# Kernel tuning notes

Hardware: AMD Instinct MI355X
Metric: run time of the kernel (lower is better)

Reference implementation:

```python
import jax, jax.numpy as jnp
import numpy as np

B, S, D, H = 2, 2048, 1024, 16
HD = D // H  # head dim 64

def setup_inputs() -> dict:
    key = jax.random.key(0)
    ks = jax.random.split(key, 12)
    s = 1.0 / np.sqrt(D)
    return {
        "query": jax.random.normal(ks[0], (B, S, D), jnp.float32),
        "key": jax.random.normal(ks[1], (B, S, D), jnp.float32),
        "value": jax.random.normal(ks[2], (B, S, D), jnp.float32),
        "Wq": jax.random.normal(ks[3], (D, D), jnp.float32) * s,
        "bq": jnp.zeros((D,), jnp.float32),
        "Wk": jax.random.normal(ks[4], (D, D), jnp.float32) * s,
        "bk": jnp.zeros((D,), jnp.float32),
        "Wv": jax.random.normal(ks[5], (D, D), jnp.float32) * s,
        "bv": jnp.zeros((D,), jnp.float32),
        "Wo": jax.random.normal(ks[6], (D, D), jnp.float32) * s,
        "bo": jnp.zeros((D,), jnp.float32),
    }

def _split_heads(x):
    # [B,S,D] -> [B,H,S,HD]
    return x.reshape(B, -1, H, HD).transpose(0, 2, 1, 3)

def reference(query, key, value, Wq, bq, Wk, bk, Wv, bv, Wo, bo):
    q = _split_heads(query @ Wq + bq)
    k = _split_heads(key @ Wk + bk)
    v = _split_heads(value @ Wv + bv)
    scale = 1.0 / np.sqrt(HD).astype(np.float32)
    scores = jnp.einsum('bhqd,bhkd->bhqk', q, k) * scale  # [B,H,S,S]
    attn = jax.nn.softmax(scores, axis=-1)
    ctx = jnp.einsum('bhqk,bhkd->bhqd', attn, v)  # [B,H,S,HD]
    ctx = ctx.transpose(0, 2, 1, 3).reshape(B, -1, D)
    out = ctx @ Wo + bo
    return out, attn
```

## Files before the change

### kernel.cpp

```cpp
#include <hip/hip_runtime.h>

#define B_ 2
#define S_ 2048
#define D_ 1024
#define H_ 16
#define HD_ 64

typedef float f32x4 __attribute__((ext_vector_type(4)));
typedef short s16x8 __attribute__((ext_vector_type(8)));

#define MFMA16(a, b, c) __builtin_amdgcn_mfma_f32_16x16x32_bf16((a), (b), (c), 0, 0, 0)

__device__ __forceinline__ unsigned short bf16_rne(float f) {
    unsigned int u = __float_as_uint(f);
    u += 0x7FFFu + ((u >> 16) & 1u);
    return (unsigned short)(u >> 16);
}
__device__ __forceinline__ float bf16_f32(unsigned short h) {
    return __uint_as_float(((unsigned int)h) << 16);
}
__device__ __forceinline__ void split_bf16(float x, short& hi, short& lo) {
    unsigned short h = bf16_rne(x);
    float r = x - bf16_f32(h);
    hi = (short)h;
    lo = (short)bf16_rne(r);
}

__global__ void wt_split_kernel(const float* __restrict__ W0, const float* __restrict__ W1,
                                const float* __restrict__ W2, const float* __restrict__ W3,
                                short* __restrict__ WtHi, short* __restrict__ WtLo) {
    int z = blockIdx.z;
    const float* W = (z == 0) ? W0 : (z == 1) ? W1 : (z == 2) ? W2 : W3;
    short* Hi = WtHi + (size_t)z * 1048576;
    short* Lo = WtLo + (size_t)z * 1048576;
    __shared__ float tile[32][33];
    int n0 = blockIdx.x * 32, k0 = blockIdx.y * 32;
    int c = threadIdx.x & 31, r = threadIdx.x >> 5;
#pragma unroll
    for (int i = 0; i < 4; i++) {
        int kl = r + i * 8;
        tile[kl][c] = W[(size_t)(k0 + kl) * D_ + n0 + c];
    }
    __syncthreads();
#pragma unroll
    for (int i = 0; i < 4; i++) {
        int nl = r + i * 8;
        float v = tile[c][nl];
        short h, l;
        split_bf16(v, h, l);
        size_t idx = (size_t)(n0 + nl) * D_ + k0 + c;
        Hi[idx] = h;
        Lo[idx] = l;
    }
}

__global__ __launch_bounds__(256) void proj_kernel(
    const float* __restrict__ Xq, const float* __restrict__ Xk, const float* __restrict__ Xv,
    const float* __restrict__ bq, const float* __restrict__ bk, const float* __restrict__ bv,
    const short* __restrict__ WtHi, const short* __restrict__ WtLo,
    short* __restrict__ Qhi, short* __restrict__ Qlo,
    short* __restrict__ Khi, short* __restrict__ Klo,
    short* __restrict__ VtHi, short* __restrict__ VtLo) {
    int z = blockIdx.z;
    const float* X = (z == 0) ? Xq : (z == 1) ? Xk : Xv;
    const float* bias = (z == 0) ? bq : (z == 1) ? bk : bv;
    const short* BH = WtHi + (size_t)z * 1048576;
    const short* BL = WtLo + (size_t)z * 1048576;
    int n0 = blockIdx.x * 64, m0 = blockIdx.y * 64;

    __shared__ alignas(16) short Ah[64][40], Al[64][40], Bh[64][40], Bl[64][40];

    int tid = threadIdx.x;
    int lane = tid & 63, w = tid >> 6;
    int wm = (w >> 1) * 32, wn = (w & 1) * 32;
    int quad = lane >> 4, l15 = lane & 15;

    f32x4 acc[2][2] = {};
    int sr = tid >> 2, scol = (tid & 3) * 8;

    for (int kb = 0; kb < 32; kb++) {
        int k0 = kb * 32;
        const float* src = X + (size_t)(m0 + sr) * D_ + k0 + scol;
        float4 f0 = *(const float4*)(src);
        float4 f1 = *(const float4*)(src + 4);
        float v[8] = {f0.x, f0.y, f0.z, f0.w, f1.x, f1.y, f1.z, f1.w};
        s16x8 hi8, lo8;
#pragma unroll
        for (int i = 0; i < 8; i++) {
            short h, l;
            split_bf16(v[i], h, l);
            hi8[i] = h;
            lo8[i] = l;
        }
        *(s16x8*)&Ah[sr][scol] = hi8;
        *(s16x8*)&Al[sr][scol] = lo8;
        *(s16x8*)&Bh[sr][scol] = *(const s16x8*)(BH + (size_t)(n0 + sr) * D_ + k0 + scol);
        *(s16x8*)&Bl[sr][scol] = *(const s16x8*)(BL + (size_t)(n0 + sr) * D_ + k0 + scol);
        __syncthreads();

        s16x8 ah[2], al[2], bh[2], bl[2];
#pragma unroll
        for (int mi = 0; mi < 2; mi++) {
            int m = wm + mi * 16 + l15;
            ah[mi] = *(const s16x8*)&Ah[m][quad * 8];
            al[mi] = *(const s16x8*)&Al[m][quad * 8];
        }
#pragma unroll
        for (int ni = 0; ni < 2; ni++) {
            int n = wn + ni * 16 + l15;
            bh[ni] = *(const s16x8*)&Bh[n][quad * 8];
            bl[ni] = *(const s16x8*)&Bl[n][quad * 8];
        }
#pragma unroll
        for (int mi = 0; mi < 2; mi++)
#pragma unroll
            for (int ni = 0; ni < 2; ni++) {
                acc[mi][ni] = MFMA16(ah[mi], bh[ni], acc[mi][ni]);
                acc[mi][ni] = MFMA16(ah[mi], bl[ni], acc[mi][ni]);
                acc[mi][ni] = MFMA16(al[mi], bh[ni], acc[mi][ni]);
            }
        __syncthreads();
    }

#pragma unroll
    for (int mi = 0; mi < 2; mi++)
#pragma unroll
        for (int ni = 0; ni < 2; ni++) {
            int nglob = n0 + wn + ni * 16 + l15;
            float bb = bias[nglob];
#pragma unroll
            for (int r = 0; r < 4; r++) {
                int mglob = m0 + wm + mi * 16 + quad * 4 + r;
                float cv = acc[mi][ni][r] + bb;
                short h, l;
                split_bf16(cv, h, l);
                if (z == 2) {
                    int bidx = mglob >> 11, s = mglob & 2047;
                    int hh = nglob >> 6, d = nglob & 63;
                    size_t idx = ((size_t)((bidx * H_ + hh) * HD_ + d)) * S_ + s;
                    VtHi[idx] = h;
                    VtLo[idx] = l;
                } else if (z == 0) {
                    size_t idx = (size_t)mglob * D_ + nglob;
                    Qhi[idx] = h;
                    Qlo[idx] = l;
                } else {
                    size_t idx = (size_t)mglob * D_ + nglob;
                    Khi[idx] = h;
                    Klo[idx] = l;
                }
            }
        }
}

__global__ __launch_bounds__(256, 2) void attn_kernel(
    const short* __restrict__ Qhi, const short* __restrict__ Qlo,
    const short* __restrict__ Khi, const short* __restrict__ Klo,
    const short* __restrict__ VtHi, const short* __restrict__ VtLo,
    float* __restrict__ attn, short* __restrict__ CtxHi, short* __restrict__ CtxLo) {
    int q0 = blockIdx.x * 16;
    int h = blockIdx.y, b = blockIdx.z;
    int tid = threadIdx.x, w = tid >> 6, lane = tid & 63;
    int quad = lane >> 4, l15 = lane & 15;

    __shared__ float redbuf[4][16];
    __shared__ float ctxbuf[4][16][64];
    __shared__ alignas(16) short Pbuf[4][2][16][40];

    size_t qrow = ((size_t)(b * S_ + q0 + l15)) * D_ + h * HD_;
    s16x8 qh[2], ql[2];
    qh[0] = *(const s16x8*)(Qhi + qrow + quad * 8);
    qh[1] = *(const s16x8*)(Qhi + qrow + 32 + quad * 8);
    ql[0] = *(const s16x8*)(Qlo + qrow + quad * 8);
    ql[1] = *(const s16x8*)(Qlo + qrow + 32 + quad * 8);

    int key_base = w * 512;
    f32x4 zero4 = {0.f, 0.f, 0.f, 0.f};
    f32x4 sc[32];
#pragma unroll
    for (int t = 0; t < 32; t++) sc[t] = zero4;

    size_t krowbase = ((size_t)(b * S_ + key_base)) * D_ + h * HD_;
#pragma unroll
    for (int kt = 0; kt < 32; kt++) {
        size_t krow = krowbase + (size_t)(kt * 16 + l15) * D_;
        s16x8 kh0 = *(const s16x8*)(Khi + krow + quad * 8);
        s16x8 kl0 = *(const s16x8*)(Klo + krow + quad * 8);
        s16x8 kh1 = *(const s16x8*)(Khi + krow + 32 + quad * 8);
        s16x8 kl1 = *(const s16x8*)(Klo + krow + 32 + quad * 8);
        f32x4 a = sc[kt];
        a = MFMA16(qh[0], kh0, a);
        a = MFMA16(qh[0], kl0, a);
        a = MFMA16(ql[0], kh0, a);
        a = MFMA16(qh[1], kh1, a);
        a = MFMA16(qh[1], kl1, a);
        a = MFMA16(ql[1], kh1, a);
        sc[kt] = a;
    }

    const float scale = 0.125f;
    float mx[4] = {-1e30f, -1e30f, -1e30f, -1e30f};
#pragma unroll
    for (int t = 0; t < 32; t++)
#pragma unroll
        for (int r = 0; r < 4; r++) {
            float v = sc[t][r] * scale;
            sc[t][r] = v;
            mx[r] = fmaxf(mx[r], v);
        }
#pragma unroll
    for (int d = 1; d < 16; d <<= 1)
#pragma unroll
        for (int r = 0; r < 4; r++) mx[r] = fmaxf(mx[r], __shfl_xor(mx[r], d));
    if (l15 == 0) {
#pragma unroll
        for (int r = 0; r < 4; r++) redbuf[w][quad * 4 + r] = mx[r];
    }
    __syncthreads();
#pragma unroll
    for (int r = 0; r < 4; r++) {
        int q = quad * 4 + r;
        mx[r] = fmaxf(fmaxf(redbuf[0][q], redbuf[1][q]), fmaxf(redbuf[2][q], redbuf[3][q]));
    }
    __syncthreads();

    float sm[4] = {0.f, 0.f, 0.f, 0.f};
#pragma unroll
    for (int t = 0; t < 32; t++)
#pragma unroll
        for (int r = 0; r < 4; r++) {
            float p = __expf(sc[t][r] - mx[r]);
            sc[t][r] = p;
            sm[r] += p;
        }
#pragma unroll
    for (int d = 1; d < 16; d <<= 1)
#pragma unroll
        for (int r = 0; r < 4; r++) sm[r] += __shfl_xor(sm[r], d);
    if (l15 == 0) {
#pragma unroll
        for (int r = 0; r < 4; r++) redbuf[w][quad * 4 + r] = sm[r];
    }
    __syncthreads();
    float rl[4];
#pragma unroll
    for (int r = 0; r < 4; r++) {
        int q = quad * 4 + r;
        float l = redbuf[0][q] + redbuf[1][q] + redbuf[2][q] + redbuf[3][q];
        rl[r] = 1.0f / l;
    }

    float* attn_base = attn + ((size_t)((b * H_ + h) * S_ + q0)) * S_ + key_base;
#pragma unroll
    for (int t = 0; t < 32; t++)
#pragma unroll
        for (int r = 0; r < 4; r++) {
            float p = sc[t][r] * rl[r];
            sc[t][r] = p;
            attn_base[(size_t)(quad * 4 + r) * S_ + t * 16 + l15] = p;
        }

    f32x4 cacc[4];
#pragma unroll
    for (int nt = 0; nt < 4; nt++) cacc[nt] = zero4;
    size_t vbase = ((size_t)((b * H_ + h) * HD_)) * S_ + key_base;
#pragma unroll
    for (int c = 0; c < 16; c++) {
#pragma unroll
        for (int tt = 0; tt < 2; tt++) {
#pragma unroll
            for (int r = 0; r < 4; r++) {
                float p = sc[2 * c + tt][r];
                short ph, pl;
                split_bf16(p, ph, pl);
                Pbuf[w][0][quad * 4 + r][tt * 16 + l15] = ph;
                Pbuf[w][1][quad * 4 + r][tt * 16 + l15] = pl;
            }
        }
        s16x8 pa_h = *(const s16x8*)&Pbuf[w][0][l15][quad * 8];
        s16x8 pa_l = *(const s16x8*)&Pbuf[w][1][l15][quad * 8];
#pragma unroll
        for (int nt = 0; nt < 4; nt++) {
            size_t vrow = vbase + (size_t)(nt * 16 + l15) * S_ + c * 32;
            s16x8 vh = *(const s16x8*)(VtHi + vrow + quad * 8);
            s16x8 vl = *(const s16x8*)(VtLo + vrow + quad * 8);
            f32x4 a = cacc[nt];
            a = MFMA16(pa_h, vh, a);
            a = MFMA16(pa_h, vl, a);
            a = MFMA16(pa_l, vh, a);
            cacc[nt] = a;
        }
    }

#pragma unroll
    for (int nt = 0; nt < 4; nt++)
#pragma unroll
        for (int r = 0; r < 4; r++) ctxbuf[w][quad * 4 + r][nt * 16 + l15] = cacc[nt][r];
    __syncthreads();
#pragma unroll
    for (int i = 0; i < 4; i++) {
        int idx = tid + i * 256;
        int q = idx >> 6, d = idx & 63;
        float cv = ctxbuf[0][q][d] + ctxbuf[1][q][d] + ctxbuf[2][q][d] + ctxbuf[3][q][d];
        short hh, ll;
        split_bf16(cv, hh, ll);
        size_t cidx = (size_t)(b * S_ + q0 + q) * D_ + h * HD_ + d;
        CtxHi[cidx] = hh;
        CtxLo[cidx] = ll;
    }
}

__global__ __launch_bounds__(256) void oproj_kernel(
    const short* __restrict__ CtxHi, const short* __restrict__ CtxLo,
    const short* __restrict__ WtHi, const short* __restrict__ WtLo,
    const float* __restrict__ bo, float* __restrict__ out) {
    const short* BH = WtHi + (size_t)3 * 1048576;
    const short* BL = WtLo + (size_t)3 * 1048576;
    int n0 = blockIdx.x * 64, m0 = blockIdx.y * 64;
    __shared__ alignas(16) short Ah[64][40], Al[64][40], Bh[64][40], Bl[64][40];
    int tid = threadIdx.x;
    int lane = tid & 63, w = tid >> 6;
    int wm = (w >> 1) * 32, wn = (w & 1) * 32;
    int quad = lane >> 4, l15 = lane & 15;
    f32x4 acc[2][2] = {};
    int sr = tid >> 2, scol = (tid & 3) * 8;

    for (int kb = 0; kb < 32; kb++) {
        int k0 = kb * 32;
        *(s16x8*)&Ah[sr][scol] = *(const s16x8*)(CtxHi + (size_t)(m0 + sr) * D_ + k0 + scol);
        *(s16x8*)&Al[sr][scol] = *(const s16x8*)(CtxLo + (size_t)(m0 + sr) * D_ + k0 + scol);
        *(s16x8*)&Bh[sr][scol] = *(const s16x8*)(BH + (size_t)(n0 + sr) * D_ + k0 + scol);
        *(s16x8*)&Bl[sr][scol] = *(const s16x8*)(BL + (size_t)(n0 + sr) * D_ + k0 + scol);
        __syncthreads();
        s16x8 ah[2], al[2], bh[2], bl[2];
#pragma unroll
        for (int mi = 0; mi < 2; mi++) {
            int m = wm + mi * 16 + l15;
            ah[mi] = *(const s16x8*)&Ah[m][quad * 8];
            al[mi] = *(const s16x8*)&Al[m][quad * 8];
        }
#pragma unroll
        for (int ni = 0; ni < 2; ni++) {
            int n = wn + ni * 16 + l15;
            bh[ni] = *(const s16x8*)&Bh[n][quad * 8];
            bl[ni] = *(const s16x8*)&Bl[n][quad * 8];
        }
#pragma unroll
        for (int mi = 0; mi < 2; mi++)
#pragma unroll
            for (int ni = 0; ni < 2; ni++) {
                acc[mi][ni] = MFMA16(ah[mi], bh[ni], acc[mi][ni]);
                acc[mi][ni] = MFMA16(ah[mi], bl[ni], acc[mi][ni]);
                acc[mi][ni] = MFMA16(al[mi], bh[ni], acc[mi][ni]);
            }
        __syncthreads();
    }
#pragma unroll
    for (int mi = 0; mi < 2; mi++)
#pragma unroll
        for (int ni = 0; ni < 2; ni++) {
            int nglob = n0 + wn + ni * 16 + l15;
            float bb = bo[nglob];
#pragma unroll
            for (int r = 0; r < 4; r++) {
                int mglob = m0 + wm + mi * 16 + quad * 4 + r;
                out[(size_t)mglob * D_ + nglob] = acc[mi][ni][r] + bb;
            }
        }
}

extern "C" void kernel_launch(void* const* d_in, const int* in_sizes, int n_in,
                              void* d_out, int out_size, void* d_ws, size_t ws_size,
                              hipStream_t stream) {
    const float* q_in = (const float*)d_in[0];
    const float* k_in = (const float*)d_in[1];
    const float* v_in = (const float*)d_in[2];
    const float* Wq = (const float*)d_in[3];
    const float* bq = (const float*)d_in[4];
    const float* Wk = (const float*)d_in[5];
    const float* bk = (const float*)d_in[6];
    const float* Wv = (const float*)d_in[7];
    const float* bv = (const float*)d_in[8];
    const float* Wo = (const float*)d_in[9];
    const float* bo = (const float*)d_in[10];

    char* ws = (char*)d_ws;
    const size_t MB8 = 8u * 1024u * 1024u;
    short* WtHi = (short*)(ws + 0 * MB8);
    short* WtLo = (short*)(ws + 1 * MB8);
    short* Qhi = (short*)(ws + 2 * MB8);
    short* Qlo = (short*)(ws + 3 * MB8);
    short* Khi = (short*)(ws + 4 * MB8);
    short* Klo = (short*)(ws + 5 * MB8);
    short* VtHi = (short*)(ws + 6 * MB8);
    short* VtLo = (short*)(ws + 7 * MB8);
    short* CtxHi = (short*)(ws + 8 * MB8);
    short* CtxLo = (short*)(ws + 9 * MB8);

    float* out = (float*)d_out;
    float* attn = out + (size_t)B_ * S_ * D_;

    wt_split_kernel<<<dim3(32, 32, 4), 256, 0, stream>>>(Wq, Wk, Wv, Wo, WtHi, WtLo);
    proj_kernel<<<dim3(16, 64, 3), 256, 0, stream>>>(q_in, k_in, v_in, bq, bk, bv,
                                                     WtHi, WtLo, Qhi, Qlo, Khi, Klo, VtHi, VtLo);
    attn_kernel<<<dim3(128, 16, 2), 256, 0, stream>>>(Qhi, Qlo, Khi, Klo, VtHi, VtLo,
                                                      attn, CtxHi, CtxLo);
    oproj_kernel<<<dim3(16, 64), 256, 0, stream>>>(CtxHi, CtxLo, WtHi, WtLo, bo, out);
}
```

Before: 1.210 ms.

## Split attention keys across 16 waves per block with swizzled block order

The attention kernel goes from 4 waves to 16 waves per block, each covering 128 keys instead of 512. This cuts score registers per thread and raises latency hiding. The block index is remapped to interleave (b,h,q) tiles across the grid, and the attn matrix is written with nontemporal stores to avoid cache pollution. The shared buffers are unioned and the context reduction becomes a two-stage tree, at the cost of more barriers and cross-wave reduction work.

```diff
diff --git a/kernel.cpp b/kernel.cpp
--- a/kernel.cpp
+++ b/kernel.cpp
@@ -153,19 +153,25 @@
         }
 }
 
-__global__ __launch_bounds__(256, 2) void attn_kernel(
+__global__ __launch_bounds__(1024, 4) void attn_kernel(
     const short* __restrict__ Qhi, const short* __restrict__ Qlo,
     const short* __restrict__ Khi, const short* __restrict__ Klo,
     const short* __restrict__ VtHi, const short* __restrict__ VtLo,
     float* __restrict__ attn, short* __restrict__ CtxHi, short* __restrict__ CtxLo) {
-    int q0 = blockIdx.x * 16;
-    int h = blockIdx.y, b = blockIdx.z;
+    int lin = blockIdx.x + 128 * (blockIdx.y + 16 * blockIdx.z);
+    int nl = (lin & 7) * 512 + (lin >> 3);
+    int q0 = (nl & 127) * 16;
+    int h = (nl >> 7) & 15;
+    int b = nl >> 11;
+
     int tid = threadIdx.x, w = tid >> 6, lane = tid & 63;
     int quad = lane >> 4, l15 = lane & 15;
 
-    __shared__ float redbuf[4][16];
-    __shared__ float ctxbuf[4][16][64];
-    __shared__ alignas(16) short Pbuf[4][2][16][40];
+    __shared__ float redbuf[16][16];
+    __shared__ alignas(16) union {
+        short P[16][2][16][40];
+        float ctx[8][16][64];
+    } sbuf;
 
     size_t qrow = ((size_t)(b * S_ + q0 + l15)) * D_ + h * HD_;
     s16x8 qh[2], ql[2];
@@ -174,15 +180,15 @@
     ql[0] = *(const s16x8*)(Qlo + qrow + quad * 8);
     ql[1] = *(const s16x8*)(Qlo + qrow + 32 + quad * 8);
 
-    int key_base = w * 512;
+    int key_base = w * 128;
     f32x4 zero4 = {0.f, 0.f, 0.f, 0.f};
-    f32x4 sc[32];
-#pragma unroll
-    for (int t = 0; t < 32; t++) sc[t] = zero4;
+    f32x4 sc[8];
+#pragma unroll
+    for (int t = 0; t < 8; t++) sc[t] = zero4;
 
     size_t krowbase = ((size_t)(b * S_ + key_base)) * D_ + h * HD_;
 #pragma unroll
-    for (int kt = 0; kt < 32; kt++) {
+    for (int kt = 0; kt < 8; kt++) {
         size_t krow = krowbase + (size_t)(kt * 16 + l15) * D_;
         s16x8 kh0 = *(const s16x8*)(Khi + krow + quad * 8);
         s16x8 kl0 = *(const s16x8*)(Klo + krow + quad * 8);
@@ -201,7 +207,7 @@
     const float scale = 0.125f;
     float mx[4] = {-1e30f, -1e30f, -1e30f, -1e30f};
 #pragma unroll
-    for (int t = 0; t < 32; t++)
+    for (int t = 0; t < 8; t++)
 #pragma unroll
         for (int r = 0; r < 4; r++) {
             float v = sc[t][r] * scale;
@@ -220,13 +226,16 @@
 #pragma unroll
     for (int r = 0; r < 4; r++) {
         int q = quad * 4 + r;
-        mx[r] = fmaxf(fmaxf(redbuf[0][q], redbuf[1][q]), fmaxf(redbuf[2][q], redbuf[3][q]));
+        float m = redbuf[0][q];
+#pragma unroll
+        for (int ww = 1; ww < 16; ww++) m = fmaxf(m, redbuf[ww][q]);
+        mx[r] = m;
     }
     __syncthreads();
 
     float sm[4] = {0.f, 0.f, 0.f, 0.f};
 #pragma unroll
-    for (int t = 0; t < 32; t++)
+    for (int t = 0; t < 8; t++)
 #pragma unroll
         for (int r = 0; r < 4; r++) {
             float p = __expf(sc[t][r] - mx[r]);
@@ -246,18 +255,20 @@
 #pragma unroll
     for (int r = 0; r < 4; r++) {
         int q = quad * 4 + r;
-        float l = redbuf[0][q] + redbuf[1][q] + redbuf[2][q] + redbuf[3][q];
+        float l = 0.f;
+#pragma unroll
+        for (int ww = 0; ww < 16; ww++) l += redbuf[ww][q];
         rl[r] = 1.0f / l;
     }
 
     float* attn_base = attn + ((size_t)((b * H_ + h) * S_ + q0)) * S_ + key_base;
 #pragma unroll
-    for (int t = 0; t < 32; t++)
+    for (int t = 0; t < 8; t++)
 #pragma unroll
         for (int r = 0; r < 4; r++) {
             float p = sc[t][r] * rl[r];
             sc[t][r] = p;
-            attn_base[(size_t)(quad * 4 + r) * S_ + t * 16 + l15] = p;
+            __builtin_nontemporal_store(p, attn_base + (size_t)(quad * 4 + r) * S_ + t * 16 + l15);
         }
 
     f32x4 cacc[4];
@@ -265,7 +276,7 @@
     for (int nt = 0; nt < 4; nt++) cacc[nt] = zero4;
     size_t vbase = ((size_t)((b * H_ + h) * HD_)) * S_ + key_base;
 #pragma unroll
-    for (int c = 0; c < 16; c++) {
+    for (int c = 0; c < 4; c++) {
 #pragma unroll
         for (int tt = 0; tt < 2; tt++) {
 #pragma unroll
@@ -273,12 +284,12 @@
                 float p = sc[2 * c + tt][r];
                 short ph, pl;
                 split_bf16(p, ph, pl);
-                Pbuf[w][0][quad * 4 + r][tt * 16 + l15] = ph;
-                Pbuf[w][1][quad * 4 + r][tt * 16 + l15] = pl;
+                sbuf.P[w][0][quad * 4 + r][tt * 16 + l15] = ph;
+                sbuf.P[w][1][quad * 4 + r][tt * 16 + l15] = pl;
             }
         }
-        s16x8 pa_h = *(const s16x8*)&Pbuf[w][0][l15][quad * 8];
-        s16x8 pa_l = *(const s16x8*)&Pbuf[w][1][l15][quad * 8];
+        s16x8 pa_h = *(const s16x8*)&sbuf.P[w][0][l15][quad * 8];
+        s16x8 pa_l = *(const s16x8*)&sbuf.P[w][1][l15][quad * 8];
 #pragma unroll
         for (int nt = 0; nt < 4; nt++) {
             size_t vrow = vbase + (size_t)(nt * 16 + l15) * S_ + c * 32;
@@ -292,16 +303,26 @@
         }
     }
 
-#pragma unroll
-    for (int nt = 0; nt < 4; nt++)
-#pragma unroll
-        for (int r = 0; r < 4; r++) ctxbuf[w][quad * 4 + r][nt * 16 + l15] = cacc[nt][r];
-    __syncthreads();
-#pragma unroll
-    for (int i = 0; i < 4; i++) {
-        int idx = tid + i * 256;
-        int q = idx >> 6, d = idx & 63;
-        float cv = ctxbuf[0][q][d] + ctxbuf[1][q][d] + ctxbuf[2][q][d] + ctxbuf[3][q][d];
+    __syncthreads();
+    if (w >= 8) {
+#pragma unroll
+        for (int nt = 0; nt < 4; nt++)
+#pragma unroll
+            for (int r = 0; r < 4; r++) sbuf.ctx[w - 8][quad * 4 + r][nt * 16 + l15] = cacc[nt][r];
+    }
+    __syncthreads();
+    if (w < 8) {
+#pragma unroll
+        for (int nt = 0; nt < 4; nt++)
+#pragma unroll
+            for (int r = 0; r < 4; r++) sbuf.ctx[w][quad * 4 + r][nt * 16 + l15] += cacc[nt][r];
+    }
+    __syncthreads();
+    {
+        int q = tid >> 6, d = tid & 63;
+        float cv = 0.f;
+#pragma unroll
+        for (int ww = 0; ww < 8; ww++) cv += sbuf.ctx[ww][q][d];
         short hh, ll;
         split_bf16(cv, hh, ll);
         size_t cidx = (size_t)(b * S_ + q0 + q) * D_ + h * HD_ + d;
@@ -403,7 +424,7 @@
     wt_split_kernel<<<dim3(32, 32, 4), 256, 0, stream>>>(Wq, Wk, Wv, Wo, WtHi, WtLo);
     proj_kernel<<<dim3(16, 64, 3), 256, 0, stream>>>(q_in, k_in, v_in, bq, bk, bv,
                                                      WtHi, WtLo, Qhi, Qlo, Khi, Klo, VtHi, VtLo);
-    attn_kernel<<<dim3(128, 16, 2), 256, 0, stream>>>(Qhi, Qlo, Khi, Klo, VtHi, VtLo,
-                                                      attn, CtxHi, CtxLo);
+    attn_kernel<<<dim3(128, 16, 2), 1024, 0, stream>>>(Qhi, Qlo, Khi, Klo, VtHi, VtLo,
+                                                       attn, CtxHi, CtxLo);
     oproj_kernel<<<dim3(16, 64), 256, 0, stream>>>(CtxHi, CtxLo, WtHi, WtLo, bo, out);
 }
```

Measured after the change: 1.235 ms. 2.1% more time.

## Transpose score MFMA layout for vectorized attn stores and remap block order

Applied to the files above, without the earlier changes.

Swaps the MFMA operands so each lane holds four consecutive keys for a single query row. The attention-probability stores become 16-byte vector writes and the P tile is written to shared memory as 4-short vectors. Per-row max and sum reductions shrink to two cross-lane shuffles on one scalar each, with separate shared buffers for max and sum. Block indices are also permuted so consecutive blocks spread across heads and batches, which changes cache and channel locality for the large attn write stream.

```diff
diff --git a/kernel.cpp b/kernel.cpp
--- a/kernel.cpp
+++ b/kernel.cpp
@@ -8,6 +8,7 @@
 
 typedef float f32x4 __attribute__((ext_vector_type(4)));
 typedef short s16x8 __attribute__((ext_vector_type(8)));
+typedef short s16x4 __attribute__((ext_vector_type(4)));
 
 #define MFMA16(a, b, c) __builtin_amdgcn_mfma_f32_16x16x32_bf16((a), (b), (c), 0, 0, 0)
 
@@ -158,12 +159,17 @@
     const short* __restrict__ Khi, const short* __restrict__ Klo,
     const short* __restrict__ VtHi, const short* __restrict__ VtLo,
     float* __restrict__ attn, short* __restrict__ CtxHi, short* __restrict__ CtxLo) {
-    int q0 = blockIdx.x * 16;
-    int h = blockIdx.y, b = blockIdx.z;
+    int lin = blockIdx.x + 128 * (blockIdx.y + 16 * blockIdx.z);
+    int nl = (lin & 7) * 512 + (lin >> 3);
+    int q0 = (nl & 127) * 16;
+    int h = (nl >> 7) & 15;
+    int b = nl >> 11;
+
     int tid = threadIdx.x, w = tid >> 6, lane = tid & 63;
     int quad = lane >> 4, l15 = lane & 15;
 
-    __shared__ float redbuf[4][16];
+    __shared__ float redmax[4][16];
+    __shared__ float redsum[4][16];
     __shared__ float ctxbuf[4][16][64];
     __shared__ alignas(16) short Pbuf[4][2][16][40];
 
@@ -189,76 +195,54 @@
         s16x8 kh1 = *(const s16x8*)(Khi + krow + 32 + quad * 8);
         s16x8 kl1 = *(const s16x8*)(Klo + krow + 32 + quad * 8);
         f32x4 a = sc[kt];
-        a = MFMA16(qh[0], kh0, a);
-        a = MFMA16(qh[0], kl0, a);
-        a = MFMA16(ql[0], kh0, a);
-        a = MFMA16(qh[1], kh1, a);
-        a = MFMA16(qh[1], kl1, a);
-        a = MFMA16(ql[1], kh1, a);
+        a = MFMA16(kh0, qh[0], a);
+        a = MFMA16(kl0, qh[0], a);
+        a = MFMA16(kh0, ql[0], a);
+        a = MFMA16(kh1, qh[1], a);
+        a = MFMA16(kl1, qh[1], a);
+        a = MFMA16(kh1, ql[1], a);
         sc[kt] = a;
     }
 
     const float scale = 0.125f;
-    float mx[4] = {-1e30f, -1e30f, -1e30f, -1e30f};
+    float mx = -1e30f;
 #pragma unroll
     for (int t = 0; t < 32; t++)
 #pragma unroll
         for (int r = 0; r < 4; r++) {
             float v = sc[t][r] * scale;
             sc[t][r] = v;
-            mx[r] = fmaxf(mx[r], v);
-        }
-#pragma unroll
-    for (int d = 1; d < 16; d <<= 1)
-#pragma unroll
-        for (int r = 0; r < 4; r++) mx[r] = fmaxf(mx[r], __shfl_xor(mx[r], d));
-    if (l15 == 0) {
-#pragma unroll
-        for (int r = 0; r < 4; r++) redbuf[w][quad * 4 + r] = mx[r];
-    }
+            mx = fmaxf(mx, v);
+        }
+    mx = fmaxf(mx, __shfl_xor(mx, 16));
+    mx = fmaxf(mx, __shfl_xor(mx, 32));
+    if (lane < 16) redmax[w][lane] = mx;
     __syncthreads();
-#pragma unroll
-    for (int r = 0; r < 4; r++) {
-        int q = quad * 4 + r;
-        mx[r] = fmaxf(fmaxf(redbuf[0][q], redbuf[1][q]), fmaxf(redbuf[2][q], redbuf[3][q]));
-    }
+    mx = fmaxf(fmaxf(redmax[0][l15], redmax[1][l15]),
+               fmaxf(redmax[2][l15], redmax[3][l15]));
+
+    float sm = 0.f;
+#pragma unroll
+    for (int t = 0; t < 32; t++)
+#pragma unroll
+        for (int r = 0; r < 4; r++) {
+            float p = __expf(sc[t][r] - mx);
+            sc[t][r] = p;
+            sm += p;
+        }
+    sm += __shfl_xor(sm, 16);
+    sm += __shfl_xor(sm, 32);
+    if (lane < 16) redsum[w][lane] = sm;
     __syncthreads();
-
-    float sm[4] = {0.f, 0.f, 0.f, 0.f};
-#pragma unroll
-    for (int t = 0; t < 32; t++)
-#pragma unroll
-        for (int r = 0; r < 4; r++) {
-            float p = __expf(sc[t][r] - mx[r]);
-            sc[t][r] = p;
-            sm[r] += p;
-        }
-#pragma unroll
-    for (int d = 1; d < 16; d <<= 1)
-#pragma unroll
-        for (int r = 0; r < 4; r++) sm[r] += __shfl_xor(sm[r], d);
-    if (l15 == 0) {
-#pragma unroll
-        for (int r = 0; r < 4; r++) redbuf[w][quad * 4 + r] = sm[r];
-    }
-    __syncthreads();
-    float rl[4];
-#pragma unroll
-    for (int r = 0; r < 4; r++) {
-        int q = quad * 4 + r;
-        float l = redbuf[0][q] + redbuf[1][q] + redbuf[2][q] + redbuf[3][q];
-        rl[r] = 1.0f / l;
-    }
+    float rl = 1.0f / (redsum[0][l15] + redsum[1][l15] + redsum[2][l15] + redsum[3][l15]);
 
     float* attn_base = attn + ((size_t)((b * H_ + h) * S_ + q0)) * S_ + key_base;
 #pragma unroll
-    for (int t = 0; t < 32; t++)
-#pragma unroll
-        for (int r = 0; r < 4; r++) {
-            float p = sc[t][r] * rl[r];
-            sc[t][r] = p;
-            attn_base[(size_t)(quad * 4 + r) * S_ + t * 16 + l15] = p;
-        }
+    for (int t = 0; t < 32; t++) {
+        f32x4 p4 = sc[t] * rl;
+        sc[t] = p4;
+        *(f32x4*)(attn_base + (size_t)l15 * S_ + t * 16 + quad * 4) = p4;
+    }
 
     f32x4 cacc[4];
 #pragma unroll
@@ -268,14 +252,17 @@
     for (int c = 0; c < 16; c++) {
 #pragma unroll
         for (int tt = 0; tt < 2; tt++) {
+            f32x4 p4 = sc[2 * c + tt];
+            s16x4 h4, l4;
 #pragma unroll
             for (int r = 0; r < 4; r++) {
-                float p = sc[2 * c + tt][r];
                 short ph, pl;
-                split_bf16(p, ph, pl);
-                Pbuf[w][0][quad * 4 + r][tt * 16 + l15] = ph;
-                Pbuf[w][1][quad * 4 + r][tt * 16 + l15] = pl;
-            }
+                split_bf16(p4[r], ph, pl);
+                h4[r] = ph;
+                l4[r] = pl;
+            }
+            *(s16x4*)&Pbuf[w][0][l15][tt * 16 + quad * 4] = h4;
+            *(s16x4*)&Pbuf[w][1][l15][tt * 16 + quad * 4] = l4;
         }
         s16x8 pa_h = *(const s16x8*)&Pbuf[w][0][l15][quad * 8];
         s16x8 pa_l = *(const s16x8*)&Pbuf[w][1][l15][quad * 8];
```

Measured after the change: 1.199 ms. Within noise of the previous version (-1.0%).
